# Optimization experiments

Measured on AMD Instinct MI355X. Metric: run time of the kernel, lower is better.

## Reference

```python
import jax, jax.numpy as jnp
import numpy as np

ROUTING_ITERS = 3

def setup_inputs() -> dict:
    key = jax.random.key(0)
    k1, k2 = jax.random.split(key)
    B, N, C, OUT, IN = 256, 1152, 10, 16, 8
    x = jax.random.normal(k1, (B, N, IN), dtype=jnp.float32)
    W = jax.random.normal(k2, (1, N, C, OUT, IN), dtype=jnp.float32)
    return {"x": x, "W": W}

def _squash_elementwise(s):
    # Faithful to original: torch.norm over trailing singleton dim == |s|,
    # so squash reduces to |s|^2/(1+|s|^2) * s/|s| = s*|s|/(1+s^2) elementwise.
    return s * jnp.abs(s) / (1.0 + s * s)

def reference(x, W):
    B = x.shape[0]
    N, C = W.shape[1], W.shape[2]
    # u_hat[b,n,k,o] = sum_i W[0,n,k,o,i] * x[b,n,i]
    u_hat = jnp.einsum('nkoi,bni->bnko', W[0], x)
    b_ij = jnp.zeros((N, C), dtype=x.dtype)  # shared across batch, as in original
    v = None
    for it in range(ROUTING_ITERS):
        c_ij = jax.nn.softmax(b_ij, axis=1)            # softmax over capsules (dim=2 orig)
        s_j = jnp.einsum('nk,bnko->bko', c_ij, u_hat)  # sum over route nodes
        v = _squash_elementwise(s_j)                    # [B, C, OUT]
        if it < ROUTING_ITERS - 1:
            # a_ij[b,n,k] = u_hat[b,n,k,:] . v[b,k,:]; mean over batch
            a = jnp.einsum('bnko,bko->nk', u_hat, v) / B
            b_ij = b_ij + a
    return v[..., None]  # [B, C, OUT, 1] matching v_j.squeeze(1)
```

## Files before the change

### kernel.cpp

```cpp
#include <hip/hip_runtime.h>
#include <math.h>

#define B 256
#define N 1152
#define C_ 10
#define OUT 16
#define IN 8
#define KO 160

#define MB 16
#define NC 9
#define NCH 128
#define KG 5
#define XSTR 84

__global__ __launch_bounds__(64, 4) void k_s_partial(
    const float* __restrict__ x, const float* __restrict__ W,
    const float* __restrict__ c, float* __restrict__ partial)
{
    __shared__ float xs[MB][XSTR];
    __shared__ float cs[NC][KG];

    const int tid = threadIdx.x;
    const int id  = blockIdx.x;
    const int g   = id & 7;
    const int q   = id >> 3;
    const int bt  = q & 15;
    const int kg  = (q >> 4) & 1;
    const int chl = q >> 5;
    const int ch  = g * 16 + chl;
    const int b0  = bt * MB;
    const int n0  = ch * NC;
    const int k0  = kg * KG;

    for (int idx = tid; idx < MB * 18; idx += 64) {
        int bl = idx / 18, r = idx - bl * 18;
        float4 val = *(const float4*)(x + (size_t)(b0 + bl) * (N * IN) + (size_t)n0 * IN + r * 4);
        *(float4*)(&xs[bl][r * 4]) = val;
    }
    if (c) {
        for (int idx = tid; idx < NC * KG; idx += 64) {
            int nl = idx / KG, kk = idx - nl * KG;
            cs[nl][kk] = c[(size_t)(n0 + nl) * C_ + (k0 + kk)];
        }
    }
    __syncthreads();

    const int o   = tid & 15;
    const int grp = (tid >> 4) * 4;

    float acc[4][KG];
#pragma unroll
    for (int r = 0; r < 4; ++r)
#pragma unroll
        for (int kk = 0; kk < KG; ++kk) acc[r][kk] = 0.f;

    const float* Wb = W + (size_t)n0 * (KO * IN) + (size_t)(k0 * OUT + o) * IN;

    for (int nl = 0; nl < NC; ++nl) {
        float4 xr[4][2];
#pragma unroll
        for (int r = 0; r < 4; ++r) {
            xr[r][0] = *(const float4*)(&xs[grp + r][nl * IN]);
            xr[r][1] = *(const float4*)(&xs[grp + r][nl * IN + 4]);
        }
        float cw[KG];
#pragma unroll
        for (int kk = 0; kk < KG; ++kk) cw[kk] = c ? cs[nl][kk] : 0.1f;

        const float* Wn = Wb + (size_t)nl * (KO * IN);
#pragma unroll
        for (int kk = 0; kk < KG; ++kk) {
            float4 w0 = *(const float4*)(Wn + kk * (OUT * IN));
            float4 w1 = *(const float4*)(Wn + kk * (OUT * IN) + 4);
#pragma unroll
            for (int r = 0; r < 4; ++r) {
                float d = w0.x * xr[r][0].x + w0.y * xr[r][0].y
                        + w0.z * xr[r][0].z + w0.w * xr[r][0].w
                        + w1.x * xr[r][1].x + w1.y * xr[r][1].y
                        + w1.z * xr[r][1].z + w1.w * xr[r][1].w;
                acc[r][kk] += cw[kk] * d;
            }
        }
    }

#pragma unroll
    for (int r = 0; r < 4; ++r) {
        float* pp = partial + (size_t)ch * (B * KO) + (size_t)(b0 + grp + r) * KO
                  + (size_t)k0 * OUT + o;
#pragma unroll
        for (int kk = 0; kk < KG; ++kk) pp[kk * OUT] = acc[r][kk];
    }
}

__global__ __launch_bounds__(256) void k_reduce_squash(
    const float* __restrict__ partial, float* __restrict__ v, float* __restrict__ out)
{
    __shared__ float red[256];
    const int tid = threadIdx.x;
    const int e   = blockIdx.x * 64 + (tid & 63);
    const int q   = tid >> 6;
    float s = 0.f;
#pragma unroll
    for (int i = 0; i < NCH / 4; ++i)
        s += partial[(size_t)(q * (NCH / 4) + i) * (B * KO) + e];
    red[tid] = s;
    __syncthreads();
    if (q == 0) {
        s = red[tid] + red[tid + 64] + red[tid + 128] + red[tid + 192];
        float vv = s * fabsf(s) / (1.f + s * s);
        v[e] = vv;
        if (out) out[e] = vv;
    }
}

__global__ __launch_bounds__(256) void k_a(
    const float* __restrict__ x, const float* __restrict__ W,
    const float* __restrict__ v, float* __restrict__ bij, int accumulate)
{
    const int n = blockIdx.x;
    const int tid = threadIdx.x;

    __shared__ float Wl[KO][IN + 1];
    __shared__ float xsl[B][IN];
    __shared__ float red[256][C_];

    for (int idx = tid; idx < KO * IN; idx += 256)
        Wl[idx >> 3][idx & 7] = W[(size_t)n * (KO * IN) + idx];
    for (int idx = tid; idx < B * IN / 4; idx += 256) {
        int bb = idx >> 1, r = idx & 1;
        *(float4*)(&xsl[bb][r * 4]) = *(const float4*)(x + (size_t)bb * (N * IN) + (size_t)n * IN + r * 4);
    }
    __syncthreads();

    const int o = tid & 15;
    const int blane = tid >> 4;

    float part[C_];
#pragma unroll
    for (int k = 0; k < C_; ++k) part[k] = 0.f;

    for (int t = 0; t < B / 16; ++t) {
        int bb = blane + t * 16;
        float xv[IN];
#pragma unroll
        for (int i = 0; i < IN; ++i) xv[i] = xsl[bb][i];
        const float* vb = v + (size_t)bb * KO + o;
#pragma unroll
        for (int k = 0; k < C_; ++k) {
            const float* wp = &Wl[k * OUT + o][0];
            float d = 0.f;
#pragma unroll
            for (int i = 0; i < IN; ++i) d += wp[i] * xv[i];
            part[k] += d * vb[k * OUT];
        }
    }

#pragma unroll
    for (int k = 0; k < C_; ++k) red[tid][k] = part[k];
    __syncthreads();
    for (int off = 128; off > 0; off >>= 1) {
        if (tid < off) {
#pragma unroll
            for (int k = 0; k < C_; ++k) red[tid][k] += red[tid + off][k];
        }
        __syncthreads();
    }
    if (tid < C_) {
        float a = red[0][tid] * (1.0f / B);
        float* bp = bij + (size_t)n * C_ + tid;
        *bp = accumulate ? (*bp + a) : a;
    }
}

__global__ __launch_bounds__(256) void k_softmax(
    const float* __restrict__ bij, float* __restrict__ c)
{
    int n = blockIdx.x * 256 + threadIdx.x;
    if (n >= N) return;
    float b[C_], m = -1e30f;
#pragma unroll
    for (int k = 0; k < C_; ++k) { b[k] = bij[(size_t)n * C_ + k]; m = fmaxf(m, b[k]); }
    float s = 0.f;
#pragma unroll
    for (int k = 0; k < C_; ++k) { float e = __expf(b[k] - m); b[k] = e; s += e; }
    float inv = 1.f / s;
#pragma unroll
    for (int k = 0; k < C_; ++k) c[(size_t)n * C_ + k] = b[k] * inv;
}

extern "C" void kernel_launch(void* const* d_in, const int* in_sizes, int n_in,
                              void* d_out, int out_size, void* d_ws, size_t ws_size,
                              hipStream_t stream)
{
    const float* x = (const float*)d_in[0];
    const float* W = (const float*)d_in[1];
    float* out = (float*)d_out;
    float* ws  = (float*)d_ws;

    float* part = ws;
    float* bij  = ws + 5242880;
    float* c    = bij + 11520;
    float* v    = c + 11520;

    const int GS = 4096;

    k_s_partial<<<GS, 64, 0, stream>>>(x, W, nullptr, part);
    k_reduce_squash<<<640, 256, 0, stream>>>(part, v, nullptr);
    k_a<<<N, 256, 0, stream>>>(x, W, v, bij, 0);

    k_softmax<<<5, 256, 0, stream>>>(bij, c);
    k_s_partial<<<GS, 64, 0, stream>>>(x, W, c, part);
    k_reduce_squash<<<640, 256, 0, stream>>>(part, v, nullptr);
    k_a<<<N, 256, 0, stream>>>(x, W, v, bij, 1);

    k_softmax<<<5, 256, 0, stream>>>(bij, c);
    k_s_partial<<<GS, 64, 0, stream>>>(x, W, c, part);
    k_reduce_squash<<<640, 256, 0, stream>>>(part, v, out);
}
```

Before: 141.2 us.

## Replace partial-sum buffers with atomic accumulation and retile routing-agreement kernel

```diff
diff --git a/kernel.cpp b/kernel.cpp
--- a/kernel.cpp
+++ b/kernel.cpp
@@ -9,14 +9,14 @@
 #define KO 160
 
 #define MB 16
-#define NC 9
-#define NCH 128
+#define NC 12
+#define NCH 96
 #define KG 5
-#define XSTR 84
+#define XSTR 100
 
 __global__ __launch_bounds__(64, 4) void k_s_partial(
     const float* __restrict__ x, const float* __restrict__ W,
-    const float* __restrict__ c, float* __restrict__ partial)
+    const float* __restrict__ c, float* __restrict__ s)
 {
     __shared__ float xs[MB][XSTR];
     __shared__ float cs[NC][KG];
@@ -28,13 +28,13 @@
     const int bt  = q & 15;
     const int kg  = (q >> 4) & 1;
     const int chl = q >> 5;
-    const int ch  = g * 16 + chl;
+    const int ch  = g * 12 + chl;
     const int b0  = bt * MB;
     const int n0  = ch * NC;
     const int k0  = kg * KG;
 
-    for (int idx = tid; idx < MB * 18; idx += 64) {
-        int bl = idx / 18, r = idx - bl * 18;
+    for (int idx = tid; idx < MB * (NC * 2); idx += 64) {
+        int bl = idx / (NC * 2), r = idx - bl * (NC * 2);
         float4 val = *(const float4*)(x + (size_t)(b0 + bl) * (N * IN) + (size_t)n0 * IN + r * 4);
         *(float4*)(&xs[bl][r * 4]) = val;
     }
@@ -58,6 +58,13 @@
     const float* Wb = W + (size_t)n0 * (KO * IN) + (size_t)(k0 * OUT + o) * IN;
 
     for (int nl = 0; nl < NC; ++nl) {
+        const float* Wn = Wb + (size_t)nl * (KO * IN);
+        float4 w[KG][2];
+#pragma unroll
+        for (int kk = 0; kk < KG; ++kk) {
+            w[kk][0] = *(const float4*)(Wn + kk * (OUT * IN));
+            w[kk][1] = *(const float4*)(Wn + kk * (OUT * IN) + 4);
+        }
         float4 xr[4][2];
 #pragma unroll
         for (int r = 0; r < 4; ++r) {
@@ -68,17 +75,14 @@
 #pragma unroll
         for (int kk = 0; kk < KG; ++kk) cw[kk] = c ? cs[nl][kk] : 0.1f;
 
-        const float* Wn = Wb + (size_t)nl * (KO * IN);
-#pragma unroll
-        for (int kk = 0; kk < KG; ++kk) {
-            float4 w0 = *(const float4*)(Wn + kk * (OUT * IN));
-            float4 w1 = *(const float4*)(Wn + kk * (OUT * IN) + 4);
+#pragma unroll
+        for (int kk = 0; kk < KG; ++kk) {
 #pragma unroll
             for (int r = 0; r < 4; ++r) {
-                float d = w0.x * xr[r][0].x + w0.y * xr[r][0].y
-                        + w0.z * xr[r][0].z + w0.w * xr[r][0].w
-                        + w1.x * xr[r][1].x + w1.y * xr[r][1].y
-                        + w1.z * xr[r][1].z + w1.w * xr[r][1].w;
+                float d = w[kk][0].x * xr[r][0].x + w[kk][0].y * xr[r][0].y
+                        + w[kk][0].z * xr[r][0].z + w[kk][0].w * xr[r][0].w
+                        + w[kk][1].x * xr[r][1].x + w[kk][1].y * xr[r][1].y
+                        + w[kk][1].z * xr[r][1].z + w[kk][1].w * xr[r][1].w;
                 acc[r][kk] += cw[kk] * d;
             }
         }
@@ -86,90 +90,94 @@
 
 #pragma unroll
     for (int r = 0; r < 4; ++r) {
-        float* pp = partial + (size_t)ch * (B * KO) + (size_t)(b0 + grp + r) * KO
-                  + (size_t)k0 * OUT + o;
-#pragma unroll
-        for (int kk = 0; kk < KG; ++kk) pp[kk * OUT] = acc[r][kk];
-    }
-}
-
-__global__ __launch_bounds__(256) void k_reduce_squash(
-    const float* __restrict__ partial, float* __restrict__ v, float* __restrict__ out)
-{
-    __shared__ float red[256];
+        float* sp = s + (size_t)(b0 + grp + r) * KO + (size_t)k0 * OUT + o;
+#pragma unroll
+        for (int kk = 0; kk < KG; ++kk)
+            atomicAdd(sp + kk * OUT, acc[r][kk]);
+    }
+}
+
+__global__ __launch_bounds__(256) void k_squash(
+    float* __restrict__ s, float* __restrict__ v, float* __restrict__ out)
+{
+    const int e = blockIdx.x * 256 + threadIdx.x;
+    float sv = s[e];
+    s[e] = 0.f;
+    float vv = sv * fabsf(sv) / (1.f + sv * sv);
+    v[e] = vv;
+    if (out) out[e] = vv;
+}
+
+__global__ __launch_bounds__(64, 4) void k_a_atomic(
+    const float* __restrict__ x, const float* __restrict__ W,
+    const float* __restrict__ v, float* __restrict__ bij)
+{
+    __shared__ float xs[MB][XSTR];
+    __shared__ float vs[MB][84];
+
     const int tid = threadIdx.x;
-    const int e   = blockIdx.x * 64 + (tid & 63);
-    const int q   = tid >> 6;
-    float s = 0.f;
-#pragma unroll
-    for (int i = 0; i < NCH / 4; ++i)
-        s += partial[(size_t)(q * (NCH / 4) + i) * (B * KO) + e];
-    red[tid] = s;
+    const int id  = blockIdx.x;
+    const int g   = id & 7;
+    const int q   = id >> 3;
+    const int bt  = q & 15;
+    const int kg  = (q >> 4) & 1;
+    const int chl = q >> 5;
+    const int ch  = g * 12 + chl;
+    const int b0  = bt * MB;
+    const int n0  = ch * NC;
+    const int k0  = kg * KG;
+
+    for (int idx = tid; idx < MB * (NC * 2); idx += 64) {
+        int bl = idx / (NC * 2), r = idx - bl * (NC * 2);
+        float4 val = *(const float4*)(x + (size_t)(b0 + bl) * (N * IN) + (size_t)n0 * IN + r * 4);
+        *(float4*)(&xs[bl][r * 4]) = val;
+    }
+    for (int idx = tid; idx < MB * (KG * 4); idx += 64) {
+        int bl = idx / (KG * 4), r = idx - bl * (KG * 4);
+        float4 val = *(const float4*)(v + (size_t)(b0 + bl) * KO + (size_t)k0 * OUT + r * 4);
+        *(float4*)(&vs[bl][r * 4]) = val;
+    }
     __syncthreads();
-    if (q == 0) {
-        s = red[tid] + red[tid + 64] + red[tid + 128] + red[tid + 192];
-        float vv = s * fabsf(s) / (1.f + s * s);
-        v[e] = vv;
-        if (out) out[e] = vv;
-    }
-}
-
-__global__ __launch_bounds__(256) void k_a(
-    const float* __restrict__ x, const float* __restrict__ W,
-    const float* __restrict__ v, float* __restrict__ bij, int accumulate)
-{
-    const int n = blockIdx.x;
-    const int tid = threadIdx.x;
-
-    __shared__ float Wl[KO][IN + 1];
-    __shared__ float xsl[B][IN];
-    __shared__ float red[256][C_];
-
-    for (int idx = tid; idx < KO * IN; idx += 256)
-        Wl[idx >> 3][idx & 7] = W[(size_t)n * (KO * IN) + idx];
-    for (int idx = tid; idx < B * IN / 4; idx += 256) {
-        int bb = idx >> 1, r = idx & 1;
-        *(float4*)(&xsl[bb][r * 4]) = *(const float4*)(x + (size_t)bb * (N * IN) + (size_t)n * IN + r * 4);
-    }
-    __syncthreads();
-
-    const int o = tid & 15;
-    const int blane = tid >> 4;
-
-    float part[C_];
-#pragma unroll
-    for (int k = 0; k < C_; ++k) part[k] = 0.f;
-
-    for (int t = 0; t < B / 16; ++t) {
-        int bb = blane + t * 16;
-        float xv[IN];
-#pragma unroll
-        for (int i = 0; i < IN; ++i) xv[i] = xsl[bb][i];
-        const float* vb = v + (size_t)bb * KO + o;
-#pragma unroll
-        for (int k = 0; k < C_; ++k) {
-            const float* wp = &Wl[k * OUT + o][0];
-            float d = 0.f;
-#pragma unroll
-            for (int i = 0; i < IN; ++i) d += wp[i] * xv[i];
-            part[k] += d * vb[k * OUT];
-        }
-    }
-
-#pragma unroll
-    for (int k = 0; k < C_; ++k) red[tid][k] = part[k];
-    __syncthreads();
-    for (int off = 128; off > 0; off >>= 1) {
-        if (tid < off) {
-#pragma unroll
-            for (int k = 0; k < C_; ++k) red[tid][k] += red[tid + off][k];
-        }
-        __syncthreads();
-    }
-    if (tid < C_) {
-        float a = red[0][tid] * (1.0f / B);
-        float* bp = bij + (size_t)n * C_ + tid;
-        *bp = accumulate ? (*bp + a) : a;
+
+    const int o   = tid & 15;
+    const int grp = (tid >> 4) * 4;
+
+    const float* Wb = W + (size_t)n0 * (KO * IN) + (size_t)(k0 * OUT + o) * IN;
+
+    for (int nl = 0; nl < NC; ++nl) {
+        const float* Wn = Wb + (size_t)nl * (KO * IN);
+        float4 w[KG][2];
+#pragma unroll
+        for (int kk = 0; kk < KG; ++kk) {
+            w[kk][0] = *(const float4*)(Wn + kk * (OUT * IN));
+            w[kk][1] = *(const float4*)(Wn + kk * (OUT * IN) + 4);
+        }
+        float4 xr[4][2];
+#pragma unroll
+        for (int r = 0; r < 4; ++r) {
+            xr[r][0] = *(const float4*)(&xs[grp + r][nl * IN]);
+            xr[r][1] = *(const float4*)(&xs[grp + r][nl * IN + 4]);
+        }
+#pragma unroll
+        for (int kk = 0; kk < KG; ++kk) {
+            float p = 0.f;
+#pragma unroll
+            for (int r = 0; r < 4; ++r) {
+                float d = w[kk][0].x * xr[r][0].x + w[kk][0].y * xr[r][0].y
+                        + w[kk][0].z * xr[r][0].z + w[kk][0].w * xr[r][0].w
+                        + w[kk][1].x * xr[r][1].x + w[kk][1].y * xr[r][1].y
+                        + w[kk][1].z * xr[r][1].z + w[kk][1].w * xr[r][1].w;
+                p += d * vs[grp + r][kk * OUT + o];
+            }
+            p += __shfl_xor(p, 1);
+            p += __shfl_xor(p, 2);
+            p += __shfl_xor(p, 4);
+            p += __shfl_xor(p, 8);
+            p += __shfl_xor(p, 16);
+            p += __shfl_xor(p, 32);
+            if (tid == 0)
+                atomicAdd(bij + (size_t)(n0 + nl) * C_ + (k0 + kk), p * (1.0f / B));
+        }
     }
 }
 
@@ -198,23 +206,25 @@
     float* out = (float*)d_out;
     float* ws  = (float*)d_ws;
 
-    float* part = ws;
-    float* bij  = ws + 5242880;
+    float* s    = ws;
+    float* bij  = ws + 40960;
     float* c    = bij + 11520;
     float* v    = c + 11520;
 
-    const int GS = 4096;
-
-    k_s_partial<<<GS, 64, 0, stream>>>(x, W, nullptr, part);
-    k_reduce_squash<<<640, 256, 0, stream>>>(part, v, nullptr);
-    k_a<<<N, 256, 0, stream>>>(x, W, v, bij, 0);
-
+    hipMemsetAsync(ws, 0, (40960 + 11520) * sizeof(float), stream);
+
+    const int GS = 3072;
+
+    k_s_partial<<<GS, 64, 0, stream>>>(x, W, nullptr, s);
+    k_squash<<<160, 256, 0, stream>>>(s, v, nullptr);
+    k_a_atomic<<<GS, 64, 0, stream>>>(x, W, v, bij);
     k_softmax<<<5, 256, 0, stream>>>(bij, c);
-    k_s_partial<<<GS, 64, 0, stream>>>(x, W, c, part);
-    k_reduce_squash<<<640, 256, 0, stream>>>(part, v, nullptr);
-    k_a<<<N, 256, 0, stream>>>(x, W, v, bij, 1);
-
+
+    k_s_partial<<<GS, 64, 0, stream>>>(x, W, c, s);
+    k_squash<<<160, 256, 0, stream>>>(s, v, nullptr);
+    k_a_atomic<<<GS, 64, 0, stream>>>(x, W, v, bij);
     k_softmax<<<5, 256, 0, stream>>>(bij, c);
-    k_s_partial<<<GS, 64, 0, stream>>>(x, W, c, part);
-    k_reduce_squash<<<640, 256, 0, stream>>>(part, v, out);
-}
+
+    k_s_partial<<<GS, 64, 0, stream>>>(x, W, c, s);
+    k_squash<<<160, 256, 0, stream>>>(s, v, out);
+}
```

Measured after the change: 171.1 us. 21.2% more time.
